# Optimization experiments

Measured on AMD Instinct MI355X. Metric: run time of the kernel, lower is better.

## Reference

```python
import jax, jax.numpy as jnp
import numpy as np

T, N, D, E, O = 2, 4096, 1024, 8, 1024

def setup_inputs() -> dict:
    key = jax.random.key(0)
    k1, k2, k3 = jax.random.split(key, 3)
    x = jax.random.normal(k1, (T, N, D), dtype=jnp.float32)
    Wg = jax.random.normal(k2, (T, D, E), dtype=jnp.float32) * (1.0 / np.sqrt(D))
    We = jax.random.normal(k3, (E, D, O), dtype=jnp.float32) * (1.0 / np.sqrt(D))
    return {"x": x, "Wg": Wg, "We": We, "k": 2}


def reference(x, Wg, We, k):
    # Per-task gating logits: [T, N, E]
    logits = jnp.einsum('tnd,tde->tne', x, Wg)
    # Top-k mask per token (scatter 1.0 at top-k indices)
    _, topk_idx = jax.lax.top_k(logits, k)                      # [T, N, k]
    mask = jax.nn.one_hot(topk_idx, E, dtype=logits.dtype).sum(-2)  # [T, N, E]
    masked = mask * logits
    gates = masked / (masked.sum(-1, keepdims=True) + 1e-9)     # [T, N, E]
    # Dense expert outputs (each expert is Linear(D, O)): [T, N, E, O]
    eout = jnp.einsum('tnd,edo->tneo', x, We)
    # Weighted combine over selected experts
    out = jnp.einsum('tne,tneo->tno', gates, eout)              # [T, N, O]
    return out
```

## Files before the change

### kernel.cpp

```cpp
#include <hip/hip_runtime.h>
#include <hip/hip_bf16.h>
#include <stdint.h>

#define T_ 2
#define N_ 4096
#define D_ 1024
#define E_ 8
#define O_ 1024

#define BM 128
#define BN 128
#define BK 32

typedef __attribute__((ext_vector_type(8))) short short8;
typedef __attribute__((ext_vector_type(4))) float f32x4;

#define AS1 __attribute__((address_space(1)))
#define AS3 __attribute__((address_space(3)))

__device__ inline void gld16(const unsigned short* g, unsigned short* l) {
    __builtin_amdgcn_global_load_lds((const AS1 unsigned int*)g,
                                     (AS3 unsigned int*)l, 16, 0, 0);
}

__device__ inline unsigned short f2bf(float f) {
    union { float f; unsigned u; } v; v.f = f;
    unsigned r = v.u + 0x7fff + ((v.u >> 16) & 1);
    return (unsigned short)(r >> 16);
}

__global__ __launch_bounds__(256) void gate_kernel(
    const float* __restrict__ x, const float* __restrict__ Wg,
    unsigned short* __restrict__ xb,
    int* __restrict__ route, float2* __restrict__ gpair)
{
    __shared__ __align__(16) float WgT[E_][D_];

    int tid = threadIdx.x;
    int wave = tid >> 6, lane = tid & 63;
    int token0 = blockIdx.x * 8;
    int t = token0 >> 12;
    const float* wgb = Wg + (size_t)t * D_ * E_;

#pragma unroll
    for (int r = 0; r < 8; ++r) {
        int f = r * 1024 + tid * 4;
        float4 v = *(const float4*)(wgb + f);
        WgT[f & 7][f >> 3]             = v.x;
        WgT[(f + 1) & 7][(f + 1) >> 3] = v.y;
        WgT[(f + 2) & 7][(f + 2) >> 3] = v.z;
        WgT[(f + 3) & 7][(f + 3) >> 3] = v.w;
    }
    __syncthreads();

#pragma unroll
    for (int tl = 0; tl < 2; ++tl) {
        int token = token0 + wave * 2 + tl;
        const float* xrow = x + (size_t)token * D_;

        float4 xv[4];
#pragma unroll
        for (int c = 0; c < 4; ++c)
            xv[c] = *(const float4*)(xrow + c * 256 + lane * 4);

        float acc[E_] = {0.f, 0.f, 0.f, 0.f, 0.f, 0.f, 0.f, 0.f};
#pragma unroll
        for (int c = 0; c < 4; ++c) {
            int d0 = c * 256 + lane * 4;
            unsigned lo = f2bf(xv[c].x) | ((unsigned)f2bf(xv[c].y) << 16);
            unsigned hi = f2bf(xv[c].z) | ((unsigned)f2bf(xv[c].w) << 16);
            *(uint2*)(&xb[(size_t)token * D_ + d0]) = make_uint2(lo, hi);
#pragma unroll
            for (int e = 0; e < E_; ++e) {
                float4 w = *(const float4*)(&WgT[e][d0]);
                acc[e] += xv[c].x * w.x + xv[c].y * w.y + xv[c].z * w.z + xv[c].w * w.w;
            }
        }
#pragma unroll
        for (int off = 1; off < 64; off <<= 1) {
#pragma unroll
            for (int e = 0; e < E_; ++e) acc[e] += __shfl_xor(acc[e], off, 64);
        }

        if (lane == 0) {
            float best = acc[0]; int bi = 0;
#pragma unroll
            for (int e = 1; e < E_; ++e) if (acc[e] > best) { best = acc[e]; bi = e; }
            float sec = -INFINITY; int si = 0;
#pragma unroll
            for (int e = 0; e < E_; ++e) if (e != bi && acc[e] > sec) { sec = acc[e]; si = e; }
            float s = best + sec + 1e-9f;
            route[token] = bi | (si << 8);
            gpair[token] = make_float2(best / s, sec / s);
        }
    }
}

__global__ __launch_bounds__(256) void build_lists(
    const int* __restrict__ route, const float2* __restrict__ gpair,
    int* __restrict__ toklist, float* __restrict__ gatelist,
    int* __restrict__ counts)
{
    int g = blockIdx.x;
    int t = g >> 3, e = g & 7;
    int tid = threadIdx.x;
    int wave = tid >> 6, lane = tid & 63;

    __shared__ int waveSum[4];
    __shared__ int base;
    if (tid == 0) base = 0;

    for (int c = 0; c < N_; c += 256) {
        int n = c + tid;
        int r = route[t * N_ + n];
        int e0 = r & 255, e1 = (r >> 8) & 255;
        bool sel = (e0 == e) || (e1 == e);
        unsigned long long b = __ballot(sel);
        int pre  = __popcll(b & ((1ull << lane) - 1ull));
        if (lane == 0) waveSum[wave] = __popcll(b);
        __syncthreads();
        int woff = 0;
#pragma unroll
        for (int w = 0; w < 4; ++w) woff += (w < wave) ? waveSum[w] : 0;
        int total = waveSum[0] + waveSum[1] + waveSum[2] + waveSum[3];
        if (sel) {
            int p = base + woff + pre;
            int slot = (e0 == e) ? 0 : 1;
            toklist[g * N_ + p] = n | (slot << 16);
            float2 gp = gpair[t * N_ + n];
            gatelist[g * N_ + p] = (e0 == e) ? gp.x : gp.y;
        }
        __syncthreads();
        if (tid == 0) base += total;
    }
    __syncthreads();
    if (tid == 0) counts[g] = base;
}

__global__ __launch_bounds__(256) void pack_kernel(
    const float* __restrict__ We, unsigned short* __restrict__ Wbp)
{
    __shared__ __align__(16) unsigned short P[64 * 136];

    int b = blockIdx.x;
    int e  = b >> 7;
    int oy = (b & 127) >> 3;
    int dz = b & 7;
    int o0 = oy * 64, d0 = dz * 128;
    int tid = threadIdx.x;

#pragma unroll
    for (int r = 0; r < 32; ++r) {
        int lin = r * 256 + tid;
        int dd = lin >> 6, oo = lin & 63;
        P[oo * 136 + dd] = f2bf(We[((size_t)(e * D_ + d0 + dd)) * O_ + o0 + oo]);
    }
    __syncthreads();

#pragma unroll
    for (int w = 0; w < 4; ++w) {
        int ci = w * 256 + tid;
        int oo = ci >> 4, dc = ci & 15;
        uint4 v = *(const uint4*)&P[oo * 136 + dc * 8];
        int o = o0 + oo;
        int ot = o >> 7, nn = o & 127;
        unsigned short* dst =
            Wbp + ((size_t)((e * 8 + ot) * 128 + nn)) * D_ + d0 + dc * 8;
        *(uint4*)dst = v;
    }
}

__global__ __launch_bounds__(256) void moe_gemm(
    const unsigned short* __restrict__ xb,
    const unsigned short* __restrict__ Wbp,
    const int* __restrict__ toklist, const float* __restrict__ gatelist,
    const int* __restrict__ counts, float* __restrict__ out)
{
    int lin = blockIdx.x;
    int mt  = lin >> 7;
    int u   = lin & 127;
    int xcd = u & 7;
    int v   = u >> 3;
    int g   = 2 * xcd + (v >> 3);
    int ot  = v & 7;
    int t   = g >> 3;

    int cnt = counts[g];
    int m0 = mt * BM;
    if (m0 >= cnt) return;

    __shared__ __align__(16) unsigned short As[BM * BK];
    __shared__ __align__(16) unsigned short Bs[BN * BK];
    __shared__ int   tokS[BM];
    __shared__ float gateS[BM];

    int tid = threadIdx.x;
    if (tid < BM) {
        int r = m0 + tid;
        tokS[tid]  = (r < cnt) ? toklist[g * N_ + r]  : -1;
        gateS[tid] = (r < cnt) ? gatelist[g * N_ + r] : 0.f;
    }
    __syncthreads();

    int wave = tid >> 6, lane = tid & 63;
    int lr = lane >> 2;
    int sg = (lane & 3) ^ (lr & 3);
    int c0 = wave * 2, c1 = c0 + 1;
    int ar0 = c0 * 16 + lr, ar1 = c1 * 16 + lr;
    int tok0 = max(tokS[ar0], 0) & 0xFFFF;
    int tok1 = max(tokS[ar1], 0) & 0xFFFF;
    const unsigned short* ag0 = xb + ((size_t)(t * N_ + tok0)) * D_ + sg * 8;
    const unsigned short* ag1 = xb + ((size_t)(t * N_ + tok1)) * D_ + sg * 8;
    const unsigned short* wb  = Wbp + ((size_t)((g & 7) * 8 + ot) * 128) * D_;
    const unsigned short* bg0 = wb + (size_t)ar0 * D_ + sg * 8;
    const unsigned short* bg1 = wb + (size_t)ar1 * D_ + sg * 8;
    unsigned short* la0 = &As[c0 * 512];
    unsigned short* la1 = &As[c1 * 512];
    unsigned short* lb0 = &Bs[c0 * 512];
    unsigned short* lb1 = &Bs[c1 * 512];

    int fr = lane & 15, q = lane >> 4;
    int wm = (wave & 1) * 64, wn = (wave >> 1) * 64;
    int fp = (q ^ (fr & 3)) * 8;

    f32x4 acc[4][4];
#pragma unroll
    for (int mi = 0; mi < 4; ++mi)
#pragma unroll
        for (int ni = 0; ni < 4; ++ni) acc[mi][ni] = (f32x4){0.f, 0.f, 0.f, 0.f};

    for (int k0 = 0; k0 < D_; k0 += BK) {
        gld16(ag0 + k0, la0);
        gld16(ag1 + k0, la1);
        gld16(bg0 + k0, lb0);
        gld16(bg1 + k0, lb1);
        __syncthreads();

        short8 af[4], bf[4];
#pragma unroll
        for (int mi = 0; mi < 4; ++mi)
            af[mi] = *(const short8*)(&As[(wm + mi * 16 + fr) * BK + fp]);
#pragma unroll
        for (int ni = 0; ni < 4; ++ni)
            bf[ni] = *(const short8*)(&Bs[(wn + ni * 16 + fr) * BK + fp]);
#pragma unroll
        for (int mi = 0; mi < 4; ++mi)
#pragma unroll
            for (int ni = 0; ni < 4; ++ni)
                acc[mi][ni] = __builtin_amdgcn_mfma_f32_16x16x32_bf16(
                    af[mi], bf[ni], acc[mi][ni], 0, 0, 0);
        __syncthreads();
    }

    float* outb = out + (size_t)t * N_ * O_;
    int ncol = ot * 128 + wn + fr;
#pragma unroll
    for (int mi = 0; mi < 4; ++mi) {
#pragma unroll
        for (int r = 0; r < 4; ++r) {
            int ml = wm + mi * 16 + q * 4 + r;
            int ent = tokS[ml];
            if (ent >= 0) {
                int tok  = ent & 0xFFFF;
                int slot = ent >> 16;
                float gate = gateS[ml];
#pragma unroll
                for (int ni = 0; ni < 4; ++ni) {
                    unsigned short* p =
                        (unsigned short*)(outb + (size_t)tok * O_ + ncol + ni * 16);
                    p[slot] = f2bf(gate * acc[mi][ni][r]);
                }
            }
        }
    }
}

__global__ __launch_bounds__(256) void combine_kernel(float* __restrict__ out)
{
    size_t i = ((size_t)blockIdx.x * 256 + threadIdx.x) * 4;
    unsigned* po = (unsigned*)out;
    uint4 v = *(uint4*)(po + i);
    float4 r;
    union { unsigned u; float f; } a, b;
#define CMB(comp, src) a.u = (src) << 16; b.u = (src) & 0xFFFF0000u; comp = a.f + b.f
    CMB(r.x, v.x); CMB(r.y, v.y); CMB(r.z, v.z); CMB(r.w, v.w);
#undef CMB
    *(float4*)(out + i) = r;
}

extern "C" void kernel_launch(void* const* d_in, const int* in_sizes, int n_in,
                              void* d_out, int out_size, void* d_ws, size_t ws_size,
                              hipStream_t stream)
{
    const float* x  = (const float*)d_in[0];
    const float* Wg = (const float*)d_in[1];
    const float* We = (const float*)d_in[2];
    float* out = (float*)d_out;

    char* ws = (char*)d_ws;
    unsigned short* xb   = (unsigned short*)(ws);
    unsigned short* Wbp  = (unsigned short*)(ws + 16777216);
    int*   toklist       = (int*)  (ws + 33554432);
    float* gatelist      = (float*)(ws + 33816576);
    int*   counts        = (int*)  (ws + 34078720);
    int*   route         = (int*)  (ws + 34078976);
    float2* gpair        = (float2*)(ws + 34111744);

    gate_kernel<<<(T_ * N_) / 8, 256, 0, stream>>>(x, Wg, xb, route, gpair);
    build_lists<<<T_ * E_, 256, 0, stream>>>(route, gpair, toklist, gatelist, counts);
    pack_kernel<<<E_ * (O_ / 64) * (D_ / 128), 256, 0, stream>>>(We, Wbp);
    moe_gemm<<<(N_ / BM) * 8 * (T_ * E_), 256, 0, stream>>>(
        xb, Wbp, toklist, gatelist, counts, out);
    combine_kernel<<<((size_t)T_ * N_ * O_) / (256 * 4), 256, 0, stream>>>(out);
}
```

Before: 196.2 us.

## Double-buffer LDS tiles in MoE GEMM, change swizzle, widen list building

Makes the grouped MoE GEMM double-buffer its A and B LDS tiles, so the global-to-LDS loads for the next K step are issued before the MFMAs on the current one, with one barrier per step instead of two. The LDS XOR swizzle is changed on both the write side (sg) and the read side (fp), which appears aimed at reducing bank conflicts. The build_lists kernel is widened to 1024 threads per block so each block needs fewer serial chunks to scan the tokens. The cost is twice the LDS for tiles, and correctness depends on the two new swizzles still matching each other.

```diff
diff --git a/kernel.cpp b/kernel.cpp
--- a/kernel.cpp
+++ b/kernel.cpp
@@ -96,7 +96,7 @@
     }
 }
 
-__global__ __launch_bounds__(256) void build_lists(
+__global__ __launch_bounds__(1024) void build_lists(
     const int* __restrict__ route, const float2* __restrict__ gpair,
     int* __restrict__ toklist, float* __restrict__ gatelist,
     int* __restrict__ counts)
@@ -106,11 +106,11 @@
     int tid = threadIdx.x;
     int wave = tid >> 6, lane = tid & 63;
 
-    __shared__ int waveSum[4];
+    __shared__ int waveSum[16];
     __shared__ int base;
     if (tid == 0) base = 0;
 
-    for (int c = 0; c < N_; c += 256) {
+    for (int c = 0; c < N_; c += 1024) {
         int n = c + tid;
         int r = route[t * N_ + n];
         int e0 = r & 255, e1 = (r >> 8) & 255;
@@ -119,10 +119,13 @@
         int pre  = __popcll(b & ((1ull << lane) - 1ull));
         if (lane == 0) waveSum[wave] = __popcll(b);
         __syncthreads();
-        int woff = 0;
-#pragma unroll
-        for (int w = 0; w < 4; ++w) woff += (w < wave) ? waveSum[w] : 0;
-        int total = waveSum[0] + waveSum[1] + waveSum[2] + waveSum[3];
+        int woff = 0, total = 0;
+#pragma unroll
+        for (int w = 0; w < 16; ++w) {
+            int s = waveSum[w];
+            total += s;
+            woff += (w < wave) ? s : 0;
+        }
         if (sel) {
             int p = base + woff + pre;
             int slot = (e0 == e) ? 0 : 1;
@@ -189,8 +192,8 @@
     int m0 = mt * BM;
     if (m0 >= cnt) return;
 
-    __shared__ __align__(16) unsigned short As[BM * BK];
-    __shared__ __align__(16) unsigned short Bs[BN * BK];
+    __shared__ __align__(16) unsigned short As[2][BM * BK];
+    __shared__ __align__(16) unsigned short Bs[2][BN * BK];
     __shared__ int   tokS[BM];
     __shared__ float gateS[BM];
 
@@ -204,7 +207,7 @@
 
     int wave = tid >> 6, lane = tid & 63;
     int lr = lane >> 2;
-    int sg = (lane & 3) ^ (lr & 3);
+    int sg = (lane & 3) ^ ((lane >> 3) & 3);
     int c0 = wave * 2, c1 = c0 + 1;
     int ar0 = c0 * 16 + lr, ar1 = c1 * 16 + lr;
     int tok0 = max(tokS[ar0], 0) & 0xFFFF;
@@ -214,14 +217,10 @@
     const unsigned short* wb  = Wbp + ((size_t)((g & 7) * 8 + ot) * 128) * D_;
     const unsigned short* bg0 = wb + (size_t)ar0 * D_ + sg * 8;
     const unsigned short* bg1 = wb + (size_t)ar1 * D_ + sg * 8;
-    unsigned short* la0 = &As[c0 * 512];
-    unsigned short* la1 = &As[c1 * 512];
-    unsigned short* lb0 = &Bs[c0 * 512];
-    unsigned short* lb1 = &Bs[c1 * 512];
 
     int fr = lane & 15, q = lane >> 4;
     int wm = (wave & 1) * 64, wn = (wave >> 1) * 64;
-    int fp = (q ^ (fr & 3)) * 8;
+    int fp = (q ^ ((fr >> 1) & 3)) * 8;
 
     f32x4 acc[4][4];
 #pragma unroll
@@ -229,28 +228,37 @@
 #pragma unroll
         for (int ni = 0; ni < 4; ++ni) acc[mi][ni] = (f32x4){0.f, 0.f, 0.f, 0.f};
 
-    for (int k0 = 0; k0 < D_; k0 += BK) {
-        gld16(ag0 + k0, la0);
-        gld16(ag1 + k0, la1);
-        gld16(bg0 + k0, lb0);
-        gld16(bg1 + k0, lb1);
-        __syncthreads();
-
-        short8 af[4], bf[4];
-#pragma unroll
-        for (int mi = 0; mi < 4; ++mi)
-            af[mi] = *(const short8*)(&As[(wm + mi * 16 + fr) * BK + fp]);
-#pragma unroll
-        for (int ni = 0; ni < 4; ++ni)
-            bf[ni] = *(const short8*)(&Bs[(wn + ni * 16 + fr) * BK + fp]);
-#pragma unroll
-        for (int mi = 0; mi < 4; ++mi)
-#pragma unroll
-            for (int ni = 0; ni < 4; ++ni)
-                acc[mi][ni] = __builtin_amdgcn_mfma_f32_16x16x32_bf16(
-                    af[mi], bf[ni], acc[mi][ni], 0, 0, 0);
-        __syncthreads();
-    }
+    gld16(ag0, &As[0][c0 * 512]);
+    gld16(ag1, &As[0][c1 * 512]);
+    gld16(bg0, &Bs[0][c0 * 512]);
+    gld16(bg1, &Bs[0][c1 * 512]);
+
+#define KSTEP(CUR, NXT, IT)                                                    \
+    {                                                                          \
+        __syncthreads();   \
+        int k1 = ((IT) + 1) * BK;                                              \
+        if (k1 < D_) {                                                         \
+            gld16(ag0 + k1, &As[NXT][c0 * 512]);                               \
+            gld16(ag1 + k1, &As[NXT][c1 * 512]);                               \
+            gld16(bg0 + k1, &Bs[NXT][c0 * 512]);                               \
+            gld16(bg1 + k1, &Bs[NXT][c1 * 512]);                               \
+        }                                                                      \
+        short8 af[4], bf[4];                                                   \
+        _Pragma("unroll") for (int mi = 0; mi < 4; ++mi)                       \
+            af[mi] = *(const short8*)(&As[CUR][(wm + mi * 16 + fr) * BK + fp]);\
+        _Pragma("unroll") for (int ni = 0; ni < 4; ++ni)                       \
+            bf[ni] = *(const short8*)(&Bs[CUR][(wn + ni * 16 + fr) * BK + fp]);\
+        _Pragma("unroll") for (int mi = 0; mi < 4; ++mi)                       \
+            _Pragma("unroll") for (int ni = 0; ni < 4; ++ni)                   \
+                acc[mi][ni] = __builtin_amdgcn_mfma_f32_16x16x32_bf16(         \
+                    af[mi], bf[ni], acc[mi][ni], 0, 0, 0);                     \
+    }
+
+    for (int it = 0; it < D_ / BK; it += 2) {
+        KSTEP(0, 1, it)
+        KSTEP(1, 0, it + 1)
+    }
+#undef KSTEP
 
     float* outb = out + (size_t)t * N_ * O_;
     int ncol = ot * 128 + wn + fr;
@@ -307,7 +315,7 @@
     float2* gpair        = (float2*)(ws + 34111744);
 
     gate_kernel<<<(T_ * N_) / 8, 256, 0, stream>>>(x, Wg, xb, route, gpair);
-    build_lists<<<T_ * E_, 256, 0, stream>>>(route, gpair, toklist, gatelist, counts);
+    build_lists<<<T_ * E_, 1024, 0, stream>>>(route, gpair, toklist, gatelist, counts);
     pack_kernel<<<E_ * (O_ / 64) * (D_ / 128), 256, 0, stream>>>(We, Wbp);
     moe_gemm<<<(N_ / BM) * 8 * (T_ * E_), 256, 0, stream>>>(
         xb, Wbp, toklist, gatelist, counts, out);
```

Measured after the change: 192.1 us. -2.1%, faster.
